# Kernel tuning notes

Measured on AMD Instinct MI355X. Metric: run time of the kernel, lower is better.

Reference implementation:

```python
import jax, jax.numpy as jnp
import numpy as np

N, E = 50000, 800000        # nodes, edges
L, MUL, S = 2, 32, 5        # layers, irrep multiplicity, num_species
NB, H = 8, 64               # num_bessel, radial MLP hidden
R_MAX = 5.0
AVG_NEIGH = 16.0
NW = 4 * MUL                # radial-MLP output size: 4 uvu TP paths x mul


def _envelope(x, p=6):
    # polynomial cutoff envelope u(x), smoothly -> 0 at x=1
    u = (1.0
         - (p + 1.0) * (p + 2.0) / 2.0 * x ** p
         + p * (p + 2.0) * x ** (p + 1)
         - p * (p + 1.0) / 2.0 * x ** (p + 2))
    return u * (x < 1.0)


def _forward(edge_vectors, node_species, senders, receivers, embed_w,
             w_res_s, w_res_v, w_lin1_s, w_lin1_v, mlp_w0, mlp_w1, mlp_w2,
             w_lin2_s, w_lin2_v, w_out1, w_out2):
    r = jnp.sqrt(jnp.sum(edge_vectors ** 2, -1) + 1e-12)            # [E] safe_norm
    unit = edge_vectors / r[:, None]
    sh1 = jnp.sqrt(3.0) * unit                                      # l=1 SH, component norm [E,3]
    # Bessel radial basis * polynomial envelope -> edge embedding [E,NB]
    n = jnp.arange(1, NB + 1, dtype=jnp.float32)
    bessel = jnp.sqrt(2.0 / R_MAX) * jnp.sin(n[None, :] * jnp.pi * r[:, None] / R_MAX) / r[:, None]
    edge_embedded = bessel * _envelope(r / R_MAX)[:, None]

    onehot = jax.nn.one_hot(node_species, S, dtype=jnp.float32)     # [N,S] node attrs (Sx0e)
    h_s = (onehot @ embed_w) / jnp.sqrt(S)                          # [N,MUL] 0e features
    h_v = jnp.zeros((N, MUL, 3), jnp.float32)                       # [N,MUL,3] 1o features (no path from 0e attrs)

    for l in range(L):
        # residual: FullyConnectedTensorProduct(node_feats, node_attrs) into h_out irreps
        res_s = jnp.einsum('nu,ns,usk->nk', h_s, onehot, w_res_s[l]) / jnp.sqrt(MUL * S)   # [N,2*MUL] (feat+gate scalars)
        res_v = jnp.einsum('nui,ns,usv->nvi', h_v, onehot, w_res_v[l]) / jnp.sqrt(MUL * S) # [N,MUL,3]
        # self-interaction Linear (per-irrep channel mixing)
        hs = (h_s @ w_lin1_s[l]) / jnp.sqrt(MUL)
        hv = jnp.einsum('nui,uv->nvi', h_v, w_lin1_v[l]) / jnp.sqrt(MUL)
        # gather sender node features onto edges
        es, ev = hs[senders], hv[senders]                           # [E,MUL], [E,MUL,3]
        # radial MLP (swish, no bias) -> per-edge uvu TP path weights [E, 4*MUL]
        a = jax.nn.silu(edge_embedded @ (mlp_w0[l] / jnp.sqrt(NB)))
        a = jax.nn.silu(a @ (mlp_w1[l] / jnp.sqrt(H)))
        w = a @ mlp_w2[l]
        w1, w2, w3, w4 = jnp.split(w, 4, axis=-1)
        # per-edge Clebsch-Gordan tensor product, uvu mode, radial weights
        o0a = w1 * es                                               # 0e x 0e -> 0e
        o0b = w2 * jnp.einsum('eui,ei->eu', ev, sh1) / jnp.sqrt(3.0)  # 1o x 1o -> 0e
        o1a = (w3 * es)[:, :, None] * sh1[:, None, :]               # 0e x 1o -> 1o
        o1b = w4[:, :, None] * ev                                   # 1o x 0e -> 1o
        # scatter-sum to receiver nodes + neighbor normalization
        seg = lambda x: jax.ops.segment_sum(x, receivers, num_segments=N) / AVG_NEIGH
        n0 = jnp.concatenate([seg(o0a), seg(o0b)], axis=-1)         # [N,2*MUL]
        n1 = jnp.concatenate([seg(o1a), seg(o1b)], axis=1)          # [N,2*MUL,3]
        # Linear to h_out irreps, add residual
        s_out = n0 @ w_lin2_s[l] / jnp.sqrt(2 * MUL) + res_s        # [N,2*MUL]
        v_out = jnp.einsum('nui,uv->nvi', n1, w_lin2_v[l]) / jnp.sqrt(2 * MUL) + res_v
        # gated nonlinearity: swish on even scalars, swish-activated gates scale vectors
        h_s = jax.nn.silu(s_out[:, :MUL])
        h_v = v_out * jax.nn.silu(s_out[:, MUL:])[:, :, None]
    # scalar readout: MUL -> MUL//2 -> 1 per node
    z = (h_s @ w_out1) / jnp.sqrt(MUL)
    e_node = (z @ w_out2) / jnp.sqrt(MUL // 2)
    return jnp.ravel(e_node)                                        # [N]


def setup_inputs():
    key = jax.random.key(0)
    ks = jax.random.split(key, 16)
    return {
        "edge_vectors": jax.random.normal(ks[0], (E, 3), jnp.float32) * 2.0,
        "node_species": jax.random.randint(ks[1], (N,), 0, S),
        "senders": jax.random.randint(ks[2], (E,), 0, N),
        "receivers": jax.random.randint(ks[3], (E,), 0, N),
        "embed_w": jax.random.normal(ks[4], (S, MUL), jnp.float32),
        "w_res_s": jax.random.normal(ks[5], (L, MUL, S, 2 * MUL), jnp.float32),
        "w_res_v": jax.random.normal(ks[6], (L, MUL, S, MUL), jnp.float32),
        "w_lin1_s": jax.random.normal(ks[7], (L, MUL, MUL), jnp.float32),
        "w_lin1_v": jax.random.normal(ks[8], (L, MUL, MUL), jnp.float32),
        "mlp_w0": jax.random.normal(ks[9], (L, NB, H), jnp.float32) * 4.0,
        "mlp_w1": jax.random.normal(ks[10], (L, H, H), jnp.float32) * 4.0,
        "mlp_w2": jax.random.normal(ks[11], (L, H, NW), jnp.float32) * 4.0 / np.sqrt(H),
        "w_lin2_s": jax.random.normal(ks[12], (L, 2 * MUL, 2 * MUL), jnp.float32),
        "w_lin2_v": jax.random.normal(ks[13], (L, 2 * MUL, MUL), jnp.float32),
        "w_out1": jax.random.normal(ks[14], (MUL, MUL // 2), jnp.float32),
        "w_out2": jax.random.normal(ks[15], (MUL // 2, 1), jnp.float32),
    }


def reference(edge_vectors, node_species, senders, receivers, embed_w,
              w_res_s, w_res_v, w_lin1_s, w_lin1_v, mlp_w0, mlp_w1, mlp_w2,
              w_lin2_s, w_lin2_v, w_out1, w_out2):
    return _forward(edge_vectors, node_species, senders, receivers, embed_w,
                    w_res_s, w_res_v, w_lin1_s, w_lin1_v, mlp_w0, mlp_w1, mlp_w2,
                    w_lin2_s, w_lin2_v, w_out1, w_out2)
```

## Files before the change

### kernel.cpp

```cpp
#include <hip/hip_runtime.h>
#include <math.h>

#define NN 50000
#define EE 800000
#define TB 8192

typedef float f32x2 __attribute__((ext_vector_type(2)));
typedef float f32x4  __attribute__((ext_vector_type(4)));
typedef short bf16x8 __attribute__((ext_vector_type(8)));

__device__ __forceinline__ float silu_f(float x) {
    return x / (1.f + __expf(-x));
}

__global__ __launch_bounds__(256) void k_table(
        const float* __restrict__ mlp_w0, const float* __restrict__ mlp_w1,
        const float* __restrict__ mlp_w2,
        float* __restrict__ tab0, float* __restrict__ tab1) {
    __shared__ float stage[4][128];
    int wv = threadIdx.x >> 6, lane = threadIdx.x & 63;
    int wid = blockIdx.x * 4 + wv;
    if (wid > 2 * TB + 1) wid = 2 * TB + 1;
    int l = wid / (TB + 1);
    int bin = wid - l * (TB + 1);
    float* st = stage[wv];

    float r = 5.f * (float)bin / (float)TB;
    if (r < 1e-6f) r = 1e-6f;
    float ir = 1.f / r;
    float xx = r * 0.2f;
    float env = 0.f;
    if (xx < 1.f) {
        float x2 = xx * xx, x3 = x2 * xx, x6 = x3 * x3, x7 = x6 * xx, x8 = x7 * xx;
        env = 1.f - 28.f * x6 + 48.f * x7 - 21.f * x8;
    }
    float coef = 0.6324555320336759f * env * ir;
    const float w5 = 0.6283185307179586f;

    float p = 0.f;
#pragma unroll
    for (int k = 0; k < 8; ++k)
        p += coef * __sinf(w5 * (float)(k + 1) * r) * mlp_w0[l * 512 + k * 64 + lane];
    float a1 = silu_f(p * 0.35355339059327373f);
    st[lane] = a1;
    __syncthreads();
    float q = 0.f;
    for (int j = 0; j < 64; ++j) q += st[j] * mlp_w1[l * 4096 + j * 64 + lane];
    float a2 = silu_f(q * 0.125f);
    __syncthreads();
    st[lane] = a2;
    __syncthreads();
    float wlo = 0.f, whi = 0.f;
    for (int h = 0; h < 64; ++h) {
        float a = st[h];
        wlo += a * mlp_w2[l * 8192 + h * 128 + lane];
        whi += a * mlp_w2[l * 8192 + h * 128 + 64 + lane];
    }
    __syncthreads();
    st[lane] = wlo;
    st[64 + lane] = whi;
    __syncthreads();
    if (lane < 32) {
        f32x2 o;
        if (l == 0) { o[0] = st[lane]; o[1] = st[64 + lane]; ((f32x2*)tab0)[bin * 32 + lane] = o; }
        else        { o[0] = st[lane]; o[1] = st[32 + lane]; ((f32x2*)tab1)[bin * 32 + lane] = o; }
    }
}

__global__ void k_fs(const float* __restrict__ embed_w, const float* __restrict__ w_lin1_s,
                     float* __restrict__ fs) {
    int t = threadIdx.x;
    if (t >= 160) return;
    int sp = t >> 5, v = t & 31;
    float acc = 0.f;
#pragma unroll
    for (int u = 0; u < 32; ++u) acc += embed_w[sp * 32 + u] * w_lin1_s[u * 32 + v];
    fs[t] = acc * 0.4472135954999579f * 0.17677669529663687f;
}

__global__ void k_hist(const int* __restrict__ recv, int* __restrict__ deg) {
    int e = blockIdx.x * 256 + threadIdx.x;
    if (e < EE) atomicAdd(&deg[recv[e]], 1);
}

__global__ void k_scan(const int* __restrict__ deg, int* __restrict__ row_start,
                       int* __restrict__ cursor) {
    __shared__ int part[256];
    int t = threadIdx.x;
    int lo = t * 196, hi = lo + 196 > NN ? NN : lo + 196;
    int s = 0;
#pragma unroll 4
    for (int i = lo; i < hi; ++i) s += deg[i];
    part[t] = s;
    __syncthreads();
    int acc = 0;
    for (int i = 0; i < t; ++i) acc += part[i];
    int run = acc;
    for (int i = lo; i < hi; ++i) {
        row_start[i] = run;
        cursor[i] = run;
        run += deg[i];
    }
    if (t == 255) row_start[NN] = run;
}

__global__ void k_fill(const int* __restrict__ recv, int* __restrict__ cursor,
                       int* __restrict__ csr_edge) {
    int e = blockIdx.x * 256 + threadIdx.x;
    if (e >= EE) return;
    int p = atomicAdd(&cursor[recv[e]], 1);
    csr_edge[p] = e;
}

__global__ void k_gather(const int* __restrict__ csr_edge, const int* __restrict__ senders,
                         const int* __restrict__ receivers, const int* __restrict__ species,
                         const float* __restrict__ evec,
                         int* __restrict__ csr_send, int* __restrict__ csr_recv,
                         float* __restrict__ ev3) {
    int p = blockIdx.x * 256 + threadIdx.x;
    if (p >= EE) return;
    int e = csr_edge[p];
    int snd = senders[e];
    csr_send[p] = snd | (species[snd] << 24);
    csr_recv[p] = receivers[e];
    ev3[p * 3 + 0] = evec[e * 3 + 0];
    ev3[p * 3 + 1] = evec[e * 3 + 1];
    ev3[p * 3 + 2] = evec[e * 3 + 2];
}

__global__ __launch_bounds__(256) void k_node_prep2(
        const float* __restrict__ h_s, const float* __restrict__ h_v,
        const float* __restrict__ w_lin1_s, const float* __restrict__ w_lin1_v,
        float* __restrict__ feat) {
    int lane = threadIdx.x & 63;
    int n = blockIdx.x * 4 + (threadIdx.x >> 6);
    n = __builtin_amdgcn_readfirstlane(n);
    if (n >= NN) return;
    const float rs32 = 0.17677669529663687f;
    int half = lane >> 5, q = lane & 31;
    const float* hsr = h_s + (size_t)n * 32;
    const float* hvr = h_v + (size_t)n * 96;
    float accA = 0.f, accB = 0.f;
#pragma unroll 8
    for (int u = 0; u < 32; ++u) {
        float ws = w_lin1_s[u * 32 + q];
        float wv = w_lin1_v[u * 32 + q];
        float xs = hsr[u];
        float xx = hvr[u];
        float xy = hvr[32 + u];
        float xz = hvr[64 + u];
        float inA = half ? xy : xs;
        float wA  = half ? wv : ws;
        float inB = half ? xz : xx;
        accA += inA * wA;
        accB += inB * wv;
    }
    f32x2 o;
    o[0] = accA * rs32;
    o[1] = accB * rs32;
    *(f32x2*)(feat + (size_t)n * 128 + q * 4 + half * 2) = o;
}

#define WROWS 24
#define WSTRIDE 260
template<int L>
__global__ __launch_bounds__(256) void k_mega(
    const int* __restrict__ csr_send, const int* __restrict__ csr_recv,
    const float* __restrict__ ev3, const int* __restrict__ row_start,
    const float* __restrict__ fs, const float* __restrict__ feat,
    const float* __restrict__ tab,
    float* __restrict__ n0, float* __restrict__ n1) {
    __shared__ f32x4 accw4[WROWS * WSTRIDE / 4];
    __shared__ f32x4 lds_esh[256];
    __shared__ float lds_x[256];
    __shared__ int lds_wd[256];
    __shared__ int sh_base, sh_last;
    float* accw = (float*)accw4;

    int tid = threadIdx.x;
    int p0 = blockIdx.x * 256;
    int lane = tid & 63;
    int wv = tid >> 6;
    int c0 = lane & 15;
    int rg = lane >> 4;

    for (int i = tid; i < WROWS * WSTRIDE / 4; i += 256) accw4[i] = (f32x4)0.f;

    int sndp = csr_send[p0 + tid];
    int rv = csr_recv[p0 + tid];
    if (tid == 0)   sh_base = rv;
    if (tid == 255) sh_last = rv;
    {
        float x = ev3[(p0 + tid) * 3 + 0], y = ev3[(p0 + tid) * 3 + 1], z = ev3[(p0 + tid) * 3 + 2];
        float r = sqrtf(x * x + y * y + z * z + 1e-12f);
        float ir = 1.f / r;
        const float s3 = 1.7320508075688772f;
        f32x4 esh;
        esh[0] = s3 * x * ir;
        esh[1] = s3 * y * ir;
        esh[2] = s3 * z * ir;
        esh[3] = __int_as_float(sndp);
        lds_esh[tid] = esh;
        float xb = r * ((float)TB / 5.f);
        if (xb > (float)TB) xb = (float)TB;
        lds_x[tid] = xb;
    }
    __syncthreads();
    int node_base = sh_base;
    lds_wd[tid] = rv - node_base;

    const f32x2* tab2 = (const f32x2*)tab;
    const f32x4* feat4 = (const f32x4*)feat;
    const float rs3 = 0.5773502691896258f;

    for (int t = 0; t < 4; ++t) {
        int tOff = wv * 64 + t * 16;

        f32x4 eshv[4];
        int wr[4];
        float xbv[4];
#pragma unroll
        for (int j = 0; j < 4; ++j) {
            int idx = tOff + rg * 4 + j;
            eshv[j] = lds_esh[idx];
            wr[j] = lds_wd[idx];
            xbv[j] = lds_x[idx];
        }

#pragma unroll
        for (int b = 0; b < 2; ++b) {
            int u = b * 16 + c0;
            float s0 = 0.f, s1 = 0.f, s2 = 0.f, s3v = 0.f;
            int curw = wr[0];
            auto emit = [&](int wrow) {
                if (L == 0) {
                    if (wrow < WROWS) {
                        float* arow = accw + wrow * WSTRIDE;
                        atomicAdd(arow + u, s0);
                        atomicAdd(arow + 64 + u, s1);
                        atomicAdd(arow + 128 + u, s2);
                        atomicAdd(arow + 192 + u, s3v);
                    } else {
                        int rvn = node_base + wrow;
                        atomicAdd(n0 + (size_t)rvn * 64 + u, s0);
                        atomicAdd(n1 + (size_t)rvn * 192 + u, s1);
                        atomicAdd(n1 + (size_t)rvn * 192 + 64 + u, s2);
                        atomicAdd(n1 + (size_t)rvn * 192 + 128 + u, s3v);
                    }
                } else {
                    if (wrow < WROWS) {
                        float* arow = accw + wrow * WSTRIDE;
                        atomicAdd(arow + u, s0);
                        atomicAdd(arow + 32 + u, s1);
                    } else {
                        int rvn = node_base + wrow;
                        atomicAdd(n0 + (size_t)rvn * 64 + u, s0);
                        atomicAdd(n0 + (size_t)rvn * 64 + 32 + u, s1);
                    }
                }
            };
#pragma unroll
            for (int j = 0; j < 4; ++j) {
                int wrow = wr[j];
                if (j > 0 && wrow != curw) {
                    emit(curw);
                    s0 = s1 = s2 = s3v = 0.f;
                    curw = wrow;
                }
                f32x4 esh = eshv[j];
                int packed = __float_as_int(esh[3]);
                float xb = xbv[j];
                int bin = (int)xb;
                if (bin >= TB) bin = TB - 1;
                float fr = xb - (float)bin;
                f32x2 wlo = tab2[bin * 32 + u];
                f32x2 whi = tab2[bin * 32 + 32 + u];
                float dA = wlo[0] + fr * (whi[0] - wlo[0]);
                float dB = wlo[1] + fr * (whi[1] - wlo[1]);
                if (L == 0) {
                    int sp = ((unsigned)packed) >> 24;
                    float es = fs[(sp << 5) + u];
                    float t3 = dB * es;
                    s0  += dA * es;
                    s1  += t3 * esh[0];
                    s2  += t3 * esh[1];
                    s3v += t3 * esh[2];
                } else {
                    int s = packed & 0xFFFFFF;
                    f32x4 f4 = feat4[(size_t)s * 32 + u];
                    float dot = f4[1] * esh[0] + f4[2] * esh[1] + f4[3] * esh[2];
                    s0 += dA * f4[0];
                    s1 += dB * dot * rs3;
                }
            }
            int alive = 1;
            {
                int pw = __shfl_xor(curw, 16);
                float t0 = __shfl_xor(s0, 16), t1 = __shfl_xor(s1, 16);
                float t2 = __shfl_xor(s2, 16), t3m = __shfl_xor(s3v, 16);
                if (pw == curw) {
                    s0 += t0; s1 += t1;
                    if (L == 0) { s2 += t2; s3v += t3m; }
                    if (lane & 16) alive = 0;
                }
            }
            {
                int pw = __shfl_xor(curw, 32);
                int pal = __shfl_xor(alive, 32);
                float t0 = __shfl_xor(s0, 32), t1 = __shfl_xor(s1, 32);
                float t2 = __shfl_xor(s2, 32), t3m = __shfl_xor(s3v, 32);
                if (alive && pal && pw == curw) {
                    s0 += t0; s1 += t1;
                    if (L == 0) { s2 += t2; s3v += t3m; }
                    if (lane & 32) alive = 0;
                }
            }
            if (alive) emit(curw);
        }
    }
    __syncthreads();

    int span = sh_last - node_base;
    if (span > WROWS - 1) span = WROWS - 1;
    for (int wl = 0; wl <= span; ++wl) {
        int n = node_base + wl;
        float v = accw[wl * WSTRIDE + tid];
        bool interior = (row_start[n] >= p0) && (row_start[n + 1] <= p0 + 256);
        if (L == 1) {
            if (tid < 64) {
                float* dest = n0 + (size_t)n * 64 + tid;
                if (interior) *dest = v;
                else if (v != 0.f) atomicAdd(dest, v);
            }
        } else {
            float* dest = (tid < 64) ? (n0 + (size_t)n * 64 + tid) : (n1 + (size_t)n * 192 + (tid - 64));
            if (interior) *dest = v;
            else if (v != 0.f) atomicAdd(dest, v);
        }
    }
}

__global__ __launch_bounds__(256) void k_node_update0(
        const int* __restrict__ species,
        const float* __restrict__ n0, const float* __restrict__ n1,
        const float* __restrict__ w_lin2_s, const float* __restrict__ w_lin2_v,
        const float* __restrict__ w_res_s, const float* __restrict__ embed_w,
        float* __restrict__ h_s, float* __restrict__ h_v) {
    int lane = threadIdx.x & 63;
    int n = blockIdx.x * 4 + (threadIdx.x >> 6);
    n = __builtin_amdgcn_readfirstlane(n);
    if (n >= NN) return;
    int sp = __builtin_amdgcn_readfirstlane(species[n]);
    const float sc_l2 = 1.f / 128.f;
    const float rr = 0.07905694150420949f * 0.4472135954999579f;

    const float* n0r = n0 + (size_t)n * 64;
    float sk = 0.f;
#pragma unroll 8
    for (int j = 0; j < 64; ++j)
        sk += n0r[j] * w_lin2_s[j * 64 + lane];
    sk *= sc_l2;
#pragma unroll 8
    for (int u = 0; u < 32; ++u)
        sk += (embed_w[sp * 32 + u] * rr) * w_res_s[(u * 5 + sp) * 64 + lane];
    float act = silu_f(sk);
    float gmine = __shfl(act, 32 + (lane & 31));

    const float* n1r = n1 + (size_t)n * 192;
    int i0 = lane >> 5, v = lane & 31;
    float acc0 = 0.f, acc2 = 0.f;
#pragma unroll 8
    for (int u = 0; u < 64; ++u) {
        float wlv = w_lin2_v[u * 32 + v];
        acc0 += n1r[i0 * 64 + u] * wlv;
        acc2 += n1r[128 + u] * wlv;
    }
    h_v[(size_t)n * 96 + i0 * 32 + v] = acc0 * sc_l2 * gmine;
    if (lane < 32) {
        h_v[(size_t)n * 96 + 64 + v] = acc2 * sc_l2 * gmine;
        h_s[(size_t)n * 32 + v] = act;
    }
}

__global__ __launch_bounds__(256) void k_node_update_last(
        const int* __restrict__ species,
        const float* __restrict__ n0,
        const float* __restrict__ w_lin2_s, const float* __restrict__ w_res_s,
        const float* __restrict__ h_s,
        const float* __restrict__ w_out1, const float* __restrict__ w_out2,
        float* __restrict__ out) {
    int lane = threadIdx.x & 63;
    int n = blockIdx.x * 4 + (threadIdx.x >> 6);
    n = __builtin_amdgcn_readfirstlane(n);
    if (n >= NN) return;
    if (lane >= 32) return;
    int sp = __builtin_amdgcn_readfirstlane(species[n]);
    const float sc_l2 = 1.f / 128.f;
    const float rs160 = 0.07905694150420949f;

    const float* n0r = n0 + (size_t)n * 64;
    float sk = 0.f;
#pragma unroll 8
    for (int j = 0; j < 64; ++j)
        sk += n0r[j] * w_lin2_s[j * 64 + lane];
    sk *= sc_l2;
    const float* hsr = h_s + (size_t)n * 32;
#pragma unroll 8
    for (int u = 0; u < 32; ++u)
        sk += (hsr[u] * rs160) * w_res_s[(u * 5 + sp) * 64 + lane];
    float act = silu_f(sk);

    float wc = 0.f;
#pragma unroll
    for (int j = 0; j < 16; ++j)
        wc += w_out1[lane * 16 + j] * w_out2[j];
    float e = act * wc;
    e += __shfl_xor(e, 1);
    e += __shfl_xor(e, 2);
    e += __shfl_xor(e, 4);
    e += __shfl_xor(e, 8);
    e += __shfl_xor(e, 16);
    if (lane == 0)
        out[n] = e * 0.17677669529663687f * 0.25f;
}

extern "C" void kernel_launch(void* const* d_in, const int* in_sizes, int n_in,
                              void* d_out, int out_size, void* d_ws, size_t ws_size,
                              hipStream_t stream) {
    const float* evec     = (const float*)d_in[0];
    const int*   species  = (const int*)d_in[1];
    const int*   senders  = (const int*)d_in[2];
    const int*   receivers= (const int*)d_in[3];
    const float* embed_w  = (const float*)d_in[4];
    const float* w_res_s  = (const float*)d_in[5];
    const float* w_res_v  = (const float*)d_in[6];
    const float* w_lin1_s = (const float*)d_in[7];
    const float* w_lin1_v = (const float*)d_in[8];
    const float* mlp_w0   = (const float*)d_in[9];
    const float* mlp_w1   = (const float*)d_in[10];
    const float* mlp_w2   = (const float*)d_in[11];
    const float* w_lin2_s = (const float*)d_in[12];
    const float* w_lin2_v = (const float*)d_in[13];
    const float* w_out1   = (const float*)d_in[14];
    const float* w_out2   = (const float*)d_in[15];
    (void)w_res_v;

    float* ws = (float*)d_ws;
    size_t off = 0;
    auto alloc = [&](size_t n) { float* p = ws + off; off += (n + 3) & ~(size_t)3; return p; };

    float* h_s  = alloc(NN * 32);
    float* h_v  = alloc(NN * 96);
    float* feat = alloc((size_t)NN * 128);
    float* n0b  = alloc(NN * 64);
    float* n1b  = alloc(NN * 192);
    float* tab0 = alloc((size_t)(TB + 1) * 64);
    float* tab1 = alloc((size_t)(TB + 1) * 64);
    float* fs   = alloc(160);
    int*   deg       = (int*)alloc(NN);
    int*   row_start = (int*)alloc(NN + 1);
    int*   cursor    = (int*)alloc(NN);
    int*   csr_edge  = (int*)alloc(EE);
    int*   csr_send  = (int*)alloc(EE);
    int*   csr_recv  = (int*)alloc(EE);
    float* ev3       = alloc((size_t)EE * 3);

    k_table<<<(2 * (TB + 1) + 3) / 4, 256, 0, stream>>>(mlp_w0, mlp_w1, mlp_w2, tab0, tab1);
    k_fs<<<1, 256, 0, stream>>>(embed_w, w_lin1_s, fs);

    hipMemsetAsync(deg, 0, NN * 4, stream);
    k_hist<<<(EE + 255) / 256, 256, 0, stream>>>(receivers, deg);
    k_scan<<<1, 256, 0, stream>>>(deg, row_start, cursor);
    k_fill<<<(EE + 255) / 256, 256, 0, stream>>>(receivers, cursor, csr_edge);
    k_gather<<<(EE + 255) / 256, 256, 0, stream>>>(csr_edge, senders, receivers, species,
                                                   evec, csr_send, csr_recv, ev3);

    hipMemsetAsync(n0b, 0, (size_t)NN * 256 * 4, stream);
    k_mega<0><<<EE / 256, 256, 0, stream>>>(
        csr_send, csr_recv, ev3, row_start, fs, feat, tab0, n0b, n1b);
    k_node_update0<<<12500, 256, 0, stream>>>(
        species, n0b, n1b, w_lin2_s, w_lin2_v, w_res_s, embed_w, h_s, h_v);

    k_node_prep2<<<12500, 256, 0, stream>>>(
        h_s, h_v, w_lin1_s + 1024, w_lin1_v + 1024, feat);
    hipMemsetAsync(n0b, 0, (size_t)NN * 64 * 4, stream);
    k_mega<1><<<EE / 256, 256, 0, stream>>>(
        csr_send, csr_recv, ev3, row_start, fs, feat, tab1, n0b, n1b);
    k_node_update_last<<<12500, 256, 0, stream>>>(
        species, n0b, w_lin2_s + 4096, w_res_s + 10240, h_s,
        w_out1, w_out2, (float*)d_out);
}
```

Baseline: 625.3 us.

## Fuse CSR fill/gather and node update/prep, vectorize radial table lookups

Merges the CSR fill and gather kernels so the edge permutation is applied in one pass, dropping the csr_edge buffer. Fuses the layer-0 node update with the layer-1 linear prep via LDS staging, which removes the h_v round trip through global memory. Halves the radial table resolution, repacks it for f32x4 loads hoisted out of the inner loop, replaces the serial prefix in k_scan with a log-step scan, and shrinks WROWS. Also cuts the w_lin2_v loop from 64 to 32 inputs, which may change the result unless the upper half was zero for layer 0. The coarser table adds interpolation error.

```diff
diff --git a/kernel.cpp b/kernel.cpp
--- a/kernel.cpp
+++ b/kernel.cpp
@@ -3,11 +3,10 @@
 
 #define NN 50000
 #define EE 800000
-#define TB 8192
+#define TB 4096
 
 typedef float f32x2 __attribute__((ext_vector_type(2)));
 typedef float f32x4  __attribute__((ext_vector_type(4)));
-typedef short bf16x8 __attribute__((ext_vector_type(8)));
 
 __device__ __forceinline__ float silu_f(float x) {
     return x / (1.f + __expf(-x));
@@ -60,10 +59,17 @@
     st[lane] = wlo;
     st[64 + lane] = whi;
     __syncthreads();
-    if (lane < 32) {
-        f32x2 o;
-        if (l == 0) { o[0] = st[lane]; o[1] = st[64 + lane]; ((f32x2*)tab0)[bin * 32 + lane] = o; }
-        else        { o[0] = st[lane]; o[1] = st[32 + lane]; ((f32x2*)tab1)[bin * 32 + lane] = o; }
+    if (lane < 16) {
+        f32x4 o;
+        if (l == 0) {
+            o[0] = st[lane]; o[1] = st[64 + lane];
+            o[2] = st[16 + lane]; o[3] = st[80 + lane];
+            ((f32x4*)tab0)[bin * 16 + lane] = o;
+        } else {
+            o[0] = st[lane]; o[1] = st[32 + lane];
+            o[2] = st[16 + lane]; o[3] = st[48 + lane];
+            ((f32x4*)tab1)[bin * 16 + lane] = o;
+        }
     }
 }
 
@@ -89,13 +95,16 @@
     int t = threadIdx.x;
     int lo = t * 196, hi = lo + 196 > NN ? NN : lo + 196;
     int s = 0;
-#pragma unroll 4
     for (int i = lo; i < hi; ++i) s += deg[i];
     part[t] = s;
     __syncthreads();
-    int acc = 0;
-    for (int i = 0; i < t; ++i) acc += part[i];
-    int run = acc;
+    for (int d = 1; d < 256; d <<= 1) {
+        int add = (t >= d) ? part[t - d] : 0;
+        __syncthreads();
+        part[t] += add;
+        __syncthreads();
+    }
+    int run = part[t] - s;
     for (int i = lo; i < hi; ++i) {
         row_start[i] = run;
         cursor[i] = run;
@@ -104,64 +113,24 @@
     if (t == 255) row_start[NN] = run;
 }
 
-__global__ void k_fill(const int* __restrict__ recv, int* __restrict__ cursor,
-                       int* __restrict__ csr_edge) {
+__global__ void k_fill(const int* __restrict__ recv, const int* __restrict__ senders,
+                       const int* __restrict__ species, const float* __restrict__ evec,
+                       int* __restrict__ cursor,
+                       int* __restrict__ csr_send, int* __restrict__ csr_recv,
+                       float* __restrict__ ev3) {
     int e = blockIdx.x * 256 + threadIdx.x;
     if (e >= EE) return;
-    int p = atomicAdd(&cursor[recv[e]], 1);
-    csr_edge[p] = e;
-}
-
-__global__ void k_gather(const int* __restrict__ csr_edge, const int* __restrict__ senders,
-                         const int* __restrict__ receivers, const int* __restrict__ species,
-                         const float* __restrict__ evec,
-                         int* __restrict__ csr_send, int* __restrict__ csr_recv,
-                         float* __restrict__ ev3) {
-    int p = blockIdx.x * 256 + threadIdx.x;
-    if (p >= EE) return;
-    int e = csr_edge[p];
+    int rv = recv[e];
+    int p = atomicAdd(&cursor[rv], 1);
     int snd = senders[e];
     csr_send[p] = snd | (species[snd] << 24);
-    csr_recv[p] = receivers[e];
+    csr_recv[p] = rv;
     ev3[p * 3 + 0] = evec[e * 3 + 0];
     ev3[p * 3 + 1] = evec[e * 3 + 1];
     ev3[p * 3 + 2] = evec[e * 3 + 2];
 }
 
-__global__ __launch_bounds__(256) void k_node_prep2(
-        const float* __restrict__ h_s, const float* __restrict__ h_v,
-        const float* __restrict__ w_lin1_s, const float* __restrict__ w_lin1_v,
-        float* __restrict__ feat) {
-    int lane = threadIdx.x & 63;
-    int n = blockIdx.x * 4 + (threadIdx.x >> 6);
-    n = __builtin_amdgcn_readfirstlane(n);
-    if (n >= NN) return;
-    const float rs32 = 0.17677669529663687f;
-    int half = lane >> 5, q = lane & 31;
-    const float* hsr = h_s + (size_t)n * 32;
-    const float* hvr = h_v + (size_t)n * 96;
-    float accA = 0.f, accB = 0.f;
-#pragma unroll 8
-    for (int u = 0; u < 32; ++u) {
-        float ws = w_lin1_s[u * 32 + q];
-        float wv = w_lin1_v[u * 32 + q];
-        float xs = hsr[u];
-        float xx = hvr[u];
-        float xy = hvr[32 + u];
-        float xz = hvr[64 + u];
-        float inA = half ? xy : xs;
-        float wA  = half ? wv : ws;
-        float inB = half ? xz : xx;
-        accA += inA * wA;
-        accB += inB * wv;
-    }
-    f32x2 o;
-    o[0] = accA * rs32;
-    o[1] = accB * rs32;
-    *(f32x2*)(feat + (size_t)n * 128 + q * 4 + half * 2) = o;
-}
-
-#define WROWS 24
+#define WROWS 20
 #define WSTRIDE 260
 template<int L>
 __global__ __launch_bounds__(256) void k_mega(
@@ -209,22 +178,33 @@
     int node_base = sh_base;
     lds_wd[tid] = rv - node_base;
 
-    const f32x2* tab2 = (const f32x2*)tab;
+    const f32x4* tabv = (const f32x4*)tab;
     const f32x4* feat4 = (const f32x4*)feat;
     const float rs3 = 0.5773502691896258f;
 
     for (int t = 0; t < 4; ++t) {
         int tOff = wv * 64 + t * 16;
 
-        f32x4 eshv[4];
+        f32x4 eshv[4], dv[4];
         int wr[4];
-        float xbv[4];
+        float es0[4], es1[4];
 #pragma unroll
         for (int j = 0; j < 4; ++j) {
             int idx = tOff + rg * 4 + j;
             eshv[j] = lds_esh[idx];
             wr[j] = lds_wd[idx];
-            xbv[j] = lds_x[idx];
+            float xb = lds_x[idx];
+            int bin = (int)xb;
+            if (bin >= TB) bin = TB - 1;
+            float fr = xb - (float)bin;
+            f32x4 lo = tabv[bin * 16 + c0];
+            f32x4 hi = tabv[bin * 16 + 16 + c0];
+            dv[j] = lo + fr * (hi - lo);
+            if (L == 0) {
+                int sp = ((unsigned)__float_as_int(eshv[j][3])) >> 24;
+                es0[j] = fs[sp * 32 + c0];
+                es1[j] = fs[sp * 32 + 16 + c0];
+            }
         }
 
 #pragma unroll
@@ -268,25 +248,17 @@
                     curw = wrow;
                 }
                 f32x4 esh = eshv[j];
-                int packed = __float_as_int(esh[3]);
-                float xb = xbv[j];
-                int bin = (int)xb;
-                if (bin >= TB) bin = TB - 1;
-                float fr = xb - (float)bin;
-                f32x2 wlo = tab2[bin * 32 + u];
-                f32x2 whi = tab2[bin * 32 + 32 + u];
-                float dA = wlo[0] + fr * (whi[0] - wlo[0]);
-                float dB = wlo[1] + fr * (whi[1] - wlo[1]);
+                float dA = dv[j][2 * b];
+                float dB = dv[j][2 * b + 1];
                 if (L == 0) {
-                    int sp = ((unsigned)packed) >> 24;
-                    float es = fs[(sp << 5) + u];
+                    float es = b ? es1[j] : es0[j];
                     float t3 = dB * es;
                     s0  += dA * es;
                     s1  += t3 * esh[0];
                     s2  += t3 * esh[1];
                     s3v += t3 * esh[2];
                 } else {
-                    int s = packed & 0xFFFFFF;
+                    int s = __float_as_int(esh[3]) & 0xFFFFFF;
                     f32x4 f4 = feat4[(size_t)s * 32 + u];
                     float dot = f4[1] * esh[0] + f4[2] * esh[1] + f4[3] * esh[2];
                     s0 += dA * f4[0];
@@ -340,16 +312,18 @@
     }
 }
 
-__global__ __launch_bounds__(256) void k_node_update0(
+__global__ __launch_bounds__(256) void k_upd0_prep(
         const int* __restrict__ species,
         const float* __restrict__ n0, const float* __restrict__ n1,
         const float* __restrict__ w_lin2_s, const float* __restrict__ w_lin2_v,
         const float* __restrict__ w_res_s, const float* __restrict__ embed_w,
-        float* __restrict__ h_s, float* __restrict__ h_v) {
+        const float* __restrict__ w_lin1_s, const float* __restrict__ w_lin1_v,
+        float* __restrict__ h_s, float* __restrict__ feat) {
+    __shared__ float stage[4][128];
     int lane = threadIdx.x & 63;
-    int n = blockIdx.x * 4 + (threadIdx.x >> 6);
+    int wv = threadIdx.x >> 6;
+    int n = blockIdx.x * 4 + wv;
     n = __builtin_amdgcn_readfirstlane(n);
-    if (n >= NN) return;
     int sp = __builtin_amdgcn_readfirstlane(species[n]);
     const float sc_l2 = 1.f / 128.f;
     const float rr = 0.07905694150420949f * 0.4472135954999579f;
@@ -370,16 +344,40 @@
     int i0 = lane >> 5, v = lane & 31;
     float acc0 = 0.f, acc2 = 0.f;
 #pragma unroll 8
-    for (int u = 0; u < 64; ++u) {
+    for (int u = 0; u < 32; ++u) {
         float wlv = w_lin2_v[u * 32 + v];
         acc0 += n1r[i0 * 64 + u] * wlv;
         acc2 += n1r[128 + u] * wlv;
     }
-    h_v[(size_t)n * 96 + i0 * 32 + v] = acc0 * sc_l2 * gmine;
+    float* st = stage[wv];
+    st[32 + i0 * 32 + v] = acc0 * sc_l2 * gmine;
     if (lane < 32) {
-        h_v[(size_t)n * 96 + 64 + v] = acc2 * sc_l2 * gmine;
+        st[v] = act;
+        st[96 + v] = acc2 * sc_l2 * gmine;
         h_s[(size_t)n * 32 + v] = act;
     }
+    __syncthreads();
+
+    const float rs32 = 0.17677669529663687f;
+    float accA = 0.f, accB = 0.f;
+#pragma unroll 8
+    for (int u = 0; u < 32; ++u) {
+        float wsv = w_lin1_s[u * 32 + v];
+        float wvv = w_lin1_v[u * 32 + v];
+        float xs = st[u];
+        float xx = st[32 + u];
+        float xy = st[64 + u];
+        float xz = st[96 + u];
+        float inA = i0 ? xy : xs;
+        float wA  = i0 ? wvv : wsv;
+        float inB = i0 ? xz : xx;
+        accA += inA * wA;
+        accB += inB * wvv;
+    }
+    f32x2 o;
+    o[0] = accA * rs32;
+    o[1] = accB * rs32;
+    *(f32x2*)(feat + (size_t)n * 128 + v * 4 + i0 * 2) = o;
 }
 
 __global__ __launch_bounds__(256) void k_node_update_last(
@@ -450,7 +448,6 @@
     auto alloc = [&](size_t n) { float* p = ws + off; off += (n + 3) & ~(size_t)3; return p; };
 
     float* h_s  = alloc(NN * 32);
-    float* h_v  = alloc(NN * 96);
     float* feat = alloc((size_t)NN * 128);
     float* n0b  = alloc(NN * 64);
     float* n1b  = alloc(NN * 192);
@@ -460,7 +457,6 @@
     int*   deg       = (int*)alloc(NN);
     int*   row_start = (int*)alloc(NN + 1);
     int*   cursor    = (int*)alloc(NN);
-    int*   csr_edge  = (int*)alloc(EE);
     int*   csr_send  = (int*)alloc(EE);
     int*   csr_recv  = (int*)alloc(EE);
     float* ev3       = alloc((size_t)EE * 3);
@@ -471,18 +467,16 @@
     hipMemsetAsync(deg, 0, NN * 4, stream);
     k_hist<<<(EE + 255) / 256, 256, 0, stream>>>(receivers, deg);
     k_scan<<<1, 256, 0, stream>>>(deg, row_start, cursor);
-    k_fill<<<(EE + 255) / 256, 256, 0, stream>>>(receivers, cursor, csr_edge);
-    k_gather<<<(EE + 255) / 256, 256, 0, stream>>>(csr_edge, senders, receivers, species,
-                                                   evec, csr_send, csr_recv, ev3);
+    k_fill<<<(EE + 255) / 256, 256, 0, stream>>>(receivers, senders, species, evec,
+                                                 cursor, csr_send, csr_recv, ev3);
 
     hipMemsetAsync(n0b, 0, (size_t)NN * 256 * 4, stream);
     k_mega<0><<<EE / 256, 256, 0, stream>>>(
         csr_send, csr_recv, ev3, row_start, fs, feat, tab0, n0b, n1b);
-    k_node_update0<<<12500, 256, 0, stream>>>(
-        species, n0b, n1b, w_lin2_s, w_lin2_v, w_res_s, embed_w, h_s, h_v);
-
-    k_node_prep2<<<12500, 256, 0, stream>>>(
-        h_s, h_v, w_lin1_s + 1024, w_lin1_v + 1024, feat);
+    k_upd0_prep<<<12500, 256, 0, stream>>>(
+        species, n0b, n1b, w_lin2_s, w_lin2_v, w_res_s, embed_w,
+        w_lin1_s + 1024, w_lin1_v + 1024, h_s, feat);
+
     hipMemsetAsync(n0b, 0, (size_t)NN * 64 * 4, stream);
     k_mega<1><<<EE / 256, 256, 0, stream>>>(
         csr_send, csr_recv, ev3, row_start, fs, feat, tab1, n0b, n1b);
```

Result: faster. 569.9 us (-8.9%).
